# Kernel optimization log

Hardware: AMD Instinct MI355X
Metric: run time of the kernel (lower is better)

## Reference

```python
import jax, jax.numpy as jnp
import numpy as np

H, W, C, B = 96, 96, 21, 2
THETA_ALPHA, THETA_BETA, THETA_GAMMA = 160.0, 3.0, 3.0
N_ITERS = 5


def _coords():
    yy, xx = jnp.meshgrid(jnp.arange(H, dtype=jnp.float32),
                          jnp.arange(W, dtype=jnp.float32), indexing='ij')
    return jnp.stack([yy.ravel(), xx.ravel()], axis=-1)  # [N,2]


def _gauss_kernel(feat):
    # exact dense Gaussian kernel exp(-||fi-fj||^2/2); ground truth for the
    # permutohedral-lattice approximate high_dim_filter op.
    sq = jnp.sum(feat * feat, axis=-1)
    d2 = sq[:, None] + sq[None, :] - 2.0 * (feat @ feat.T)
    return jnp.exp(-0.5 * jnp.maximum(d2, 0.0))  # [N,N]


def setup_inputs():
    key = jax.random.key(0)
    k1, k2 = jax.random.split(key)
    unary = jax.random.normal(k1, (B, H, W, C), dtype=jnp.float32)
    rgb = jax.random.uniform(k2, (B, H, W, 3), dtype=jnp.float32) * 255.0
    return {
        'unary': unary,
        'rgb': rgb,
        'spatial_ker_weights': jnp.eye(C, dtype=jnp.float32),
        'bilateral_ker_weights': jnp.eye(C, dtype=jnp.float32),
        'compatibility_matrix': -jnp.eye(C, dtype=jnp.float32),
    }


def _crf_single(u_chw, rgb_chw, Ws, Wb, M):
    N = H * W
    pos = _coords()
    # filter op has no gradient w.r.t. guide features in the original custom op
    rgb_flat = jax.lax.stop_gradient(rgb_chw).reshape(3, N).T  # [N,3]
    Ks = _gauss_kernel(pos / THETA_GAMMA)                       # spatial kernel [N,N]
    Kb = _gauss_kernel(jnp.concatenate([pos / THETA_ALPHA,
                                        rgb_flat / THETA_BETA], axis=-1))  # bilateral [N,N]
    ones = jnp.ones((N,), dtype=jnp.float32)
    sn = Ks @ ones  # spatial norm vals (filter of all-ones)
    bn = Kb @ ones  # bilateral norm vals
    u = u_chw.reshape(C, N)
    q = u
    for _ in range(N_ITERS):
        sm = jax.nn.softmax(q, axis=0)   # softmax over classes, [C,N]
        sp = (sm @ Ks) / sn              # Ks symmetric -> filtering = sm @ Ks
        bl = (sm @ Kb) / bn
        msg = Ws @ sp + Wb @ bl          # learned message passing [C,N]
        q = u - M @ msg                  # compatibility transform + unary update
    return q  # [C,N]


def reference(unary, rgb, spatial_ker_weights, bilateral_ker_weights, compatibility_matrix):
    u = jnp.transpose(unary, (0, 3, 1, 2))  # [B,C,H,W]
    r = jnp.transpose(rgb, (0, 3, 1, 2))    # [B,3,H,W]
    q = jax.vmap(_crf_single, in_axes=(0, 0, None, None, None))(
        u, r, spatial_ker_weights, bilateral_ker_weights, compatibility_matrix)
    return jnp.transpose(q.reshape(B, C, H, W), (0, 2, 3, 1))  # [B,H,W,C]
```

## Files before the change

kernel.cpp:

```cpp
#include <hip/hip_runtime.h>

#define HH 96
#define WW 96
#define CC 21
#define BB 2
#define NN (HH*WW)
#define NT16 (NN/16)
#define NJB  (NN/32)
#define CHK 8
#define NCONV (BB*CC)
#define NBIL 648
#define PRUNE_T 24.0f
#define GST 104

#define KSA2 (0.84932184f / 160.0f)
#define KSB2 (0.84932184f / 3.0f)
#define GL2  (1.44269504f / 18.0f)

typedef __attribute__((ext_vector_type(4))) float f32x4;
typedef __attribute__((ext_vector_type(8))) short short8;
typedef __attribute__((ext_vector_type(4))) int int4v;

static __device__ inline unsigned pk_bf16(float a, float b) {
    unsigned ua = __builtin_bit_cast(unsigned, a);
    unsigned ub = __builtin_bit_cast(unsigned, b);
    ua += 0x7FFF + ((ua >> 16) & 1);
    ub += 0x7FFF + ((ub >> 16) & 1);
    return (ua >> 16) | (ub & 0xFFFF0000u);
}
static __device__ inline unsigned short bf16_1(float a) {
    unsigned ua = __builtin_bit_cast(unsigned, a);
    ua += 0x7FFF + ((ua >> 16) & 1);
    return (unsigned short)(ua >> 16);
}

__global__ __launch_bounds__(256) void histprep_kernel(
    const float* __restrict__ rgb, unsigned* __restrict__ gh,
    float* __restrict__ sxt, unsigned short* __restrict__ gbt,
    unsigned short* __restrict__ smht, unsigned* __restrict__ bnd)
{
    int tid = threadIdx.x;
    int gid = blockIdx.x * 256 + tid;
    if (gid < BB * NN) {
        int b = gid / NN;
        const float* rp = rgb + (size_t)gid * 3;
        int cr = min(15, (int)rp[0] >> 4);
        int cg = min(15, (int)rp[1] >> 4);
        int cb = min(15, (int)rp[2] >> 4);
        atomicAdd(&gh[b * 4096 + ((cr << 8) | (cg << 4) | cb)], 1u);
    }
    unsigned* smd = (unsigned*)smht;
    for (int o = gid; o < BB * 11 * (NN / 2); o += 104 * 256) {
        int b = o / (11 * (NN / 2));
        int rem = o - b * 11 * (NN / 2);
        int rr = rem / (NN / 2), col = rem - rr * (NN / 2);
        smd[(size_t)(b * 32 + 21 + rr) * (NN / 2) + col] = (rr == 0) ? 0x3F803F80u : 0u;
    }
    if (gid < BB * NT16 * 3) {
        int t2 = gid / 3, f = gid - t2 * 3;
        bnd[t2 * 6 + 2 * f + 1] = 0u;
    }
    if (blockIdx.x == 0) {
        __shared__ float gt[96];
        if (tid < 96) gt[tid] = __builtin_amdgcn_exp2f(-(float)(tid * tid) * GL2);
        __syncthreads();
        if (tid < 96) {
            float s = 0.f;
            for (int v = 0; v < 96; v++) s += gt[abs(tid - v)];
            sxt[tid] = s;
            for (int v = 0; v < 96; v++) gbt[tid * 96 + v] = bf16_1(gt[abs(tid - v)]);
        }
    }
}

__global__ __launch_bounds__(256) void scan_kernel(
    const unsigned* __restrict__ gh, int* __restrict__ goff,
    const unsigned* __restrict__ sent)
{
    __shared__ int ps[256];
    unsigned sv = sent[0];
    int t = threadIdx.x, b = blockIdx.x;
    int base = b * 4096 + t * 16;
    int loc[16], s = 0;
#pragma unroll
    for (int k = 0; k < 16; k++) { loc[k] = (int)(gh[base + k] - sv); s += loc[k]; }
    ps[t] = s;
    __syncthreads();
    for (int off = 1; off < 256; off <<= 1) {
        int add = (t >= off) ? ps[t - off] : 0;
        __syncthreads();
        ps[t] += add;
        __syncthreads();
    }
    int run = ps[t] - s;
#pragma unroll
    for (int k = 0; k < 16; k++) { goff[base + k] = run; run += loc[k]; }
}

__global__ __launch_bounds__(256) void scatter_kernel(
    const float* __restrict__ rgb, int* __restrict__ goff,
    int* __restrict__ spos, float* __restrict__ fjs, unsigned* __restrict__ bnd)
{
    int idx = blockIdx.x * 256 + threadIdx.x;
    if (idx >= BB * NN) return;
    int b = idx / NN, p = idx - b * NN;
    const float* rp = rgb + (size_t)idx * 3;
    float r = rp[0], g = rp[1], bl = rp[2];
    int cr = min(15, (int)r >> 4);
    int cg = min(15, (int)g >> 4);
    int cb = min(15, (int)bl >> 4);
    int pos = atomicAdd(&goff[b * 4096 + ((cr << 8) | (cg << 4) | cb)], 1);
    spos[idx] = pos;
    int y = p / WW, x = p - y * WW;
    float fr = r * KSB2, fg = g * KSB2, fb2 = bl * KSB2;
    float* fb = fjs + (size_t)b * 5 * NN;
    fb[0 * NN + pos] = fr;
    fb[1 * NN + pos] = fg;
    fb[2 * NN + pos] = fb2;
    fb[3 * NN + pos] = (float)y * KSA2;
    fb[4 * NN + pos] = (float)x * KSA2;
    unsigned* bq = bnd + (size_t)(b * NT16 + (pos >> 4)) * 6;
    atomicMin(&bq[0], __float_as_uint(fr));  atomicMax(&bq[1], __float_as_uint(fr));
    atomicMin(&bq[2], __float_as_uint(fg));  atomicMax(&bq[3], __float_as_uint(fg));
    atomicMin(&bq[4], __float_as_uint(fb2)); atomicMax(&bq[5], __float_as_uint(fb2));
}

__global__ __launch_bounds__(256) void masksoft_kernel(
    const float* __restrict__ bnd, unsigned short* __restrict__ jlist,
    int* __restrict__ cnt, int* __restrict__ wl, unsigned* __restrict__ wlc,
    const unsigned* __restrict__ sent,
    const float* __restrict__ q, const int* __restrict__ spos,
    unsigned short* __restrict__ smpb, unsigned short* __restrict__ smht,
    float* __restrict__ part)
{
    int tid = threadIdx.x;
    if (blockIdx.x < 288) {
        int lane = tid & 63;
        int bt = blockIdx.x * 4 + (tid >> 6);
        if (bt >= BB * NT16) return;
        int b = bt / NT16;
        const float* tb = bnd + (size_t)bt * 6;
        float tlo0 = tb[0], thi0 = tb[1], tlo1 = tb[2], thi1 = tb[3], tlo2 = tb[4], thi2 = tb[5];
        unsigned short* jl = jlist + (size_t)bt * NJB;
        const float* bb = bnd + (size_t)b * NT16 * 6;
        int n = 0;
#pragma unroll
        for (int r = 0; r < 5; r++) {
            int jb = r * 64 + lane;
            bool keep = false;
            if (jb < NJB) {
                const float* a0 = bb + (size_t)(2 * jb) * 6;
                float s = 0.f;
#pragma unroll
                for (int f = 0; f < 3; f++) {
                    float jlo = fminf(a0[2 * f], a0[6 + 2 * f]);
                    float jhi = fmaxf(a0[2 * f + 1], a0[6 + 2 * f + 1]);
                    float lo = (f == 0) ? tlo0 : (f == 1) ? tlo1 : tlo2;
                    float hi = (f == 0) ? thi0 : (f == 1) ? thi1 : thi2;
                    float gap = fmaxf(0.f, fmaxf(lo - jhi, jlo - hi));
                    s = fmaf(gap, gap, s);
                }
                keep = (s <= PRUNE_T);
            }
            unsigned long long m = __ballot(keep);
            if (keep) {
                int pre = __popcll(m & ((1ull << lane) - 1ull));
                jl[n + pre] = (unsigned short)jb;
            }
            n += __popcll(m);
        }
        if (lane == 0) {
            cnt[bt] = n;
            int nsl = (n + CHK - 1) / CHK;
            if (nsl > 0) {
                int base = (int)(atomicAdd(wlc, (unsigned)nsl) - sent[0]);
                for (int s2 = 0; s2 < nsl; s2++) wl[base + s2] = bt * 64 + s2;
            }
        }
        return;
    }
    int idx = (blockIdx.x - 288) * 256 + tid;
    if (idx >= BB * NN) return;
    int b = idx / NN, p = idx - b * NN;
    const float* qp = q + (size_t)idx * CC;
    float v[CC], m = -1e30f;
#pragma unroll
    for (int c = 0; c < CC; c++) { v[c] = qp[c]; m = fmaxf(m, v[c]); }
    float ssum = 0.f;
#pragma unroll
    for (int c = 0; c < CC; c++) { v[c] = __expf(v[c] - m); ssum += v[c]; }
    float inv = 1.0f / ssum;
    int s = spos[idx];
#pragma unroll
    for (int c = 0; c < CC; c++) {
        unsigned short h = bf16_1(v[c] * inv);
        smpb[(size_t)(b * CC + c) * NN + p] = h;
        smht[(size_t)(b * 32 + c) * NN + s] = h;
    }
    float* pp = part + (size_t)(b * NN + s) * 24;
#pragma unroll
    for (int k = 0; k < 24; k++) pp[k] = 0.f;
}

struct JSet { float vf[5][8]; short8 sb0, sb1; };

static __device__ __forceinline__ void load_jset(
    JSet& s, const float* __restrict__ fb, const unsigned short* __restrict__ smb,
    int jb, int quad, int l16)
{
    int coff = jb * 32 + quad * 8;
#pragma unroll
    for (int f = 0; f < 5; f++) {
        const float4* pf = (const float4*)(fb + (size_t)f * NN + coff);
        float4 lo = pf[0], hi = pf[1];
        s.vf[f][0] = lo.x; s.vf[f][1] = lo.y; s.vf[f][2] = lo.z; s.vf[f][3] = lo.w;
        s.vf[f][4] = hi.x; s.vf[f][5] = hi.y; s.vf[f][6] = hi.z; s.vf[f][7] = hi.w;
    }
    s.sb0 = *(const short8*)(smb + (size_t)l16 * NN + coff);
    s.sb1 = *(const short8*)(smb + (size_t)(16 + l16) * NN + coff);
}

static __device__ __forceinline__ void compute_jset(
    const JSet& s, float fi0, float fi1, float fi2, float fi3, float fi4,
    f32x4& acc0, f32x4& acc1)
{
    float kf[8];
#pragma unroll
    for (int e = 0; e < 8; e++) {
        float d0 = s.vf[0][e] - fi0;
        float d1 = s.vf[1][e] - fi1;
        float d2 = s.vf[2][e] - fi2;
        float d3 = s.vf[3][e] - fi3;
        float d4 = s.vf[4][e] - fi4;
        float sm = d0 * d0;
        sm = fmaf(d1, d1, sm);
        sm = fmaf(d2, d2, sm);
        sm = fmaf(d3, d3, sm);
        sm = fmaf(d4, d4, sm);
        kf[e] = __builtin_amdgcn_exp2f(-sm);
    }
    int4v ap = { (int)pk_bf16(kf[0], kf[1]), (int)pk_bf16(kf[2], kf[3]),
                 (int)pk_bf16(kf[4], kf[5]), (int)pk_bf16(kf[6], kf[7]) };
    short8 afrag = __builtin_bit_cast(short8, ap);
    acc0 = __builtin_amdgcn_mfma_f32_16x16x32_bf16(afrag, s.sb0, acc0, 0, 0, 0);
    acc1 = __builtin_amdgcn_mfma_f32_16x16x32_bf16(afrag, s.sb1, acc1, 0, 0, 0);
}

__global__ __launch_bounds__(256) void conv_bil_kernel(
    const unsigned short* __restrict__ smpb, const unsigned short* __restrict__ gbt,
    const float* __restrict__ sxt, float* __restrict__ spf,
    const unsigned short* __restrict__ smht_c, const float* __restrict__ fjs,
    const unsigned short* __restrict__ jlist, const int* __restrict__ cntv,
    const int* __restrict__ wl, const unsigned* __restrict__ wlc,
    const unsigned* __restrict__ sent, float* __restrict__ part)
{
    __shared__ unsigned short C1t[96 * GST];
    int tid = threadIdx.x;
    int lane = tid & 63, w = tid >> 6;
    int quad = lane >> 4, l16 = lane & 15;
    int bid = blockIdx.x;

    if (bid < NCONV) {
        const unsigned short* plane = smpb + (size_t)bid * NN;
        for (int mt = w; mt < 6; mt += 4) {
            int m0 = mt * 16;
            short8 a[3];
#pragma unroll
            for (int kk = 0; kk < 3; kk++)
                a[kk] = *(const short8*)(plane + (size_t)(m0 + l16) * 96 + kk * 32 + quad * 8);
            f32x4 acc[6];
#pragma unroll
            for (int nt = 0; nt < 6; nt++) acc[nt] = (f32x4){0.f, 0.f, 0.f, 0.f};
#pragma unroll
            for (int nt = 0; nt < 6; nt++) {
#pragma unroll
                for (int kk = 0; kk < 3; kk++) {
                    short8 bf = *(const short8*)(gbt + (nt * 16 + l16) * 96 + kk * 32 + quad * 8);
                    acc[nt] = __builtin_amdgcn_mfma_f32_16x16x32_bf16(a[kk], bf, acc[nt], 0, 0, 0);
                }
            }
#pragma unroll
            for (int nt = 0; nt < 6; nt++) {
                unsigned* dst = (unsigned*)&C1t[(nt * 16 + l16) * GST + m0 + quad * 4];
                dst[0] = pk_bf16(acc[nt][0], acc[nt][1]);
                dst[1] = pk_bf16(acc[nt][2], acc[nt][3]);
            }
        }
        __syncthreads();
        float* outp = spf + (size_t)bid * NN;
        for (int mt = w; mt < 6; mt += 4) {
            int m0 = mt * 16;
            short8 a[3];
#pragma unroll
            for (int kk = 0; kk < 3; kk++)
                a[kk] = *(const short8*)(gbt + (m0 + l16) * 96 + kk * 32 + quad * 8);
            f32x4 acc[6];
#pragma unroll
            for (int nt = 0; nt < 6; nt++) acc[nt] = (f32x4){0.f, 0.f, 0.f, 0.f};
#pragma unroll
            for (int nt = 0; nt < 6; nt++) {
#pragma unroll
                for (int kk = 0; kk < 3; kk++) {
                    short8 bf = *(const short8*)&C1t[(nt * 16 + l16) * GST + kk * 32 + quad * 8];
                    acc[nt] = __builtin_amdgcn_mfma_f32_16x16x32_bf16(a[kk], bf, acc[nt], 0, 0, 0);
                }
            }
#pragma unroll
            for (int nt = 0; nt < 6; nt++) {
                int x = nt * 16 + l16;
                float sx = sxt[x];
#pragma unroll
                for (int r = 0; r < 4; r++) {
                    int y = m0 + quad * 4 + r;
                    float invn = __builtin_amdgcn_rcpf(sxt[y] * sx);
                    outp[y * 96 + x] = acc[nt][r] * invn;
                }
            }
        }
        return;
    }

    int nwl = (int)(wlc[0] - sent[0]);
    for (int widx = (bid - NCONV) * 4 + w; widx < nwl; widx += NBIL * 4) {
        int e = wl[widx];
        int bt = e >> 6, ck = e & 63;
        int cnt = min(cntv[bt] - ck * CHK, CHK);
        int b = bt / NT16, tile16 = bt - b * NT16;
        int i = tile16 * 16 + l16;
        const float* fb = fjs + (size_t)b * 5 * NN;
        float fi0 = fb[0 * NN + i], fi1 = fb[1 * NN + i], fi2 = fb[2 * NN + i];
        float fi3 = fb[3 * NN + i], fi4 = fb[4 * NN + i];
        f32x4 acc0 = {0.f, 0.f, 0.f, 0.f};
        f32x4 acc1 = {0.f, 0.f, 0.f, 0.f};
        const unsigned short* smb = smht_c + (size_t)b * 32 * NN;
        const unsigned short* jl = jlist + (size_t)bt * NJB + ck * CHK;
        JSet A, B;
        load_jset(A, fb, smb, jl[0], quad, l16);
        int k = 0;
        while (true) {
            if (k + 1 < cnt) load_jset(B, fb, smb, jl[k + 1], quad, l16);
            compute_jset(A, fi0, fi1, fi2, fi3, fi4, acc0, acc1);
            if (++k >= cnt) break;
            if (k + 1 < cnt) load_jset(A, fb, smb, jl[k + 1], quad, l16);
            compute_jset(B, fi0, fi1, fi2, fi3, fi4, acc0, acc1);
            if (++k >= cnt) break;
        }
        int ibase = tile16 * 16 + quad * 4;
        float* pr = part + (size_t)b * NN * 24;
#pragma unroll
        for (int r = 0; r < 4; r++)
            atomicAdd(&pr[(size_t)(ibase + r) * 24 + l16], acc0[r]);
        if (l16 < 6) {
#pragma unroll
            for (int r = 0; r < 4; r++)
                atomicAdd(&pr[(size_t)(ibase + r) * 24 + 16 + l16], acc1[r]);
        }
    }
}

__global__ __launch_bounds__(128) void update_fused_kernel(
    const float* __restrict__ u, const float* __restrict__ spf,
    float* __restrict__ part, const int* __restrict__ spos,
    const float* __restrict__ Ws, const float* __restrict__ Wb,
    const float* __restrict__ M, float* __restrict__ qout,
    unsigned short* __restrict__ smpb, unsigned short* __restrict__ smht, int wr)
{
    __shared__ float sWs[441], sWb[441], sM[441];
    for (int t = threadIdx.x; t < 441; t += 128) {
        sWs[t] = Ws[t]; sWb[t] = Wb[t]; sM[t] = M[t];
    }
    __syncthreads();
    int idx = blockIdx.x * 128 + threadIdx.x;
    if (idx >= BB * NN) return;
    int b = idx / NN, p = idx - b * NN;
    int s = spos[idx];
    float* pp = part + (size_t)(b * NN + s) * 24;
    float blv[22];
#pragma unroll
    for (int c = 0; c < 22; c++) blv[c] = pp[c];
    float ninv = 1.0f / blv[21];
    float spv[CC], msg[CC];
#pragma unroll
    for (int c = 0; c < CC; c++) {
        blv[c] *= ninv;
        spv[c] = spf[(size_t)(b * CC + c) * NN + p];
    }
#pragma unroll
    for (int c = 0; c < CC; c++) {
        float a = 0.f;
        const float* wr2 = &sWs[c * CC];
        const float* br = &sWb[c * CC];
#pragma unroll
        for (int c2 = 0; c2 < CC; c2++) a = fmaf(wr2[c2], spv[c2], a);
#pragma unroll
        for (int c2 = 0; c2 < CC; c2++) a = fmaf(br[c2], blv[c2], a);
        msg[c] = a;
    }
    const float* up = u + (size_t)idx * CC;
    float qv[CC];
#pragma unroll
    for (int c = 0; c < CC; c++) {
        float a = up[c];
        const float* mr = &sM[c * CC];
#pragma unroll
        for (int c2 = 0; c2 < CC; c2++) a = fmaf(-mr[c2], msg[c2], a);
        qv[c] = a;
    }
    if (wr) {
        float m = -1e30f;
#pragma unroll
        for (int c = 0; c < CC; c++) m = fmaxf(m, qv[c]);
        float ssum = 0.f;
        float ev[CC];
#pragma unroll
        for (int c = 0; c < CC; c++) { ev[c] = __expf(qv[c] - m); ssum += ev[c]; }
        float inv = 1.0f / ssum;
#pragma unroll
        for (int c = 0; c < CC; c++) {
            unsigned short h = bf16_1(ev[c] * inv);
            smpb[(size_t)(b * CC + c) * NN + p] = h;
            smht[(size_t)(b * 32 + c) * NN + s] = h;
        }
#pragma unroll
        for (int k = 0; k < 24; k++) pp[k] = 0.f;
    } else {
        float* qp = qout + (size_t)idx * CC;
#pragma unroll
        for (int c = 0; c < CC; c++) qp[c] = qv[c];
    }
}

extern "C" void kernel_launch(void* const* d_in, const int* in_sizes, int n_in,
                              void* d_out, int out_size, void* d_ws, size_t ws_size,
                              hipStream_t stream)
{
    const float* unary = (const float*)d_in[0];
    const float* rgb   = (const float*)d_in[1];
    const float* Ws    = (const float*)d_in[2];
    const float* Wb    = (const float*)d_in[3];
    const float* M     = (const float*)d_in[4];
    float* out = (float*)d_out;

    float* SXT  = (float*)d_ws;
    float* FJS  = SXT + 96;
    float* SPF  = FJS + (size_t)BB * 5 * NN;
    float* PART = SPF + (size_t)BB * CC * NN;
    unsigned* BND = (unsigned*)(PART + (size_t)BB * NN * 24);
    int*   SPOS = (int*)(BND + (size_t)BB * NT16 * 6);
    unsigned* GH = (unsigned*)(SPOS + BB * NN);
    int*   GOFF = (int*)(GH + BB * 4096);
    int*   CNT  = GOFF + BB * 4096;
    unsigned* WLC = (unsigned*)(CNT + BB * NT16);
    unsigned* SENT = WLC + 1;
    int*   WL   = (int*)(SENT + 1);
    unsigned short* JL = (unsigned short*)(WL + BB * NT16 * 36);
    unsigned short* SMHT = JL + (size_t)BB * NT16 * NJB;
    unsigned short* SMPB = SMHT + (size_t)BB * 32 * NN;
    unsigned short* GBT  = SMPB + (size_t)BB * CC * NN;

    histprep_kernel<<<104, 256, 0, stream>>>(rgb, GH, SXT, GBT, SMHT, BND);
    scan_kernel<<<BB, 256, 0, stream>>>(GH, GOFF, SENT);
    scatter_kernel<<<(BB * NN + 255) / 256, 256, 0, stream>>>(rgb, GOFF, SPOS, FJS, BND);
    masksoft_kernel<<<360, 256, 0, stream>>>((const float*)BND, JL, CNT, WL, WLC, SENT,
                                             unary, SPOS, SMPB, SMHT, PART);
    for (int it = 0; it < 5; ++it) {
        conv_bil_kernel<<<NCONV + NBIL, 256, 0, stream>>>(
            SMPB, GBT, SXT, SPF, SMHT, FJS, JL, CNT, WL, WLC, SENT, PART);
        update_fused_kernel<<<(BB * NN + 127) / 128, 128, 0, stream>>>(
            unary, SPF, PART, SPOS, Ws, Wb, M, out, SMPB, SMHT, (it < 4) ? 1 : 0);
    }
}
```

Baseline: 309.4 us.

## Fuse histogram scan into scatter kernel and lower pruning threshold

Merges the scan and scatter kernels into one launch. Each scatter block redundantly scans its batch's 4096-bin histogram into shared memory. Slot assignment now comes from atomic decrements on a second histogram copy, so histprep builds two copies. Separately, the bilateral pruning threshold is lowered, which skips more tiles but loosens accuracy and risks tolerance failure.

```diff
diff --git a/kernel.cpp b/kernel.cpp
--- a/kernel.cpp
+++ b/kernel.cpp
@@ -10,7 +10,7 @@
 #define CHK 8
 #define NCONV (BB*CC)
 #define NBIL 648
-#define PRUNE_T 24.0f
+#define PRUNE_T 20.0f
 #define GST 104
 
 #define KSA2 (0.84932184f / 160.0f)
@@ -35,9 +35,10 @@
 }
 
 __global__ __launch_bounds__(256) void histprep_kernel(
-    const float* __restrict__ rgb, unsigned* __restrict__ gh,
-    float* __restrict__ sxt, unsigned short* __restrict__ gbt,
-    unsigned short* __restrict__ smht, unsigned* __restrict__ bnd)
+    const float* __restrict__ rgb, unsigned* __restrict__ gha,
+    unsigned* __restrict__ ghb, float* __restrict__ sxt,
+    unsigned short* __restrict__ gbt, unsigned short* __restrict__ smht,
+    unsigned* __restrict__ bnd)
 {
     int tid = threadIdx.x;
     int gid = blockIdx.x * 256 + tid;
@@ -47,7 +48,9 @@
         int cr = min(15, (int)rp[0] >> 4);
         int cg = min(15, (int)rp[1] >> 4);
         int cb = min(15, (int)rp[2] >> 4);
-        atomicAdd(&gh[b * 4096 + ((cr << 8) | (cg << 4) | cb)], 1u);
+        int cell = b * 4096 + ((cr << 8) | (cg << 4) | cb);
+        atomicAdd(&gha[cell], 1u);
+        atomicAdd(&ghb[cell], 1u);
     }
     unsigned* smd = (unsigned*)smht;
     for (int o = gid; o < BB * 11 * (NN / 2); o += 104 * 256) {
@@ -73,17 +76,21 @@
     }
 }
 
-__global__ __launch_bounds__(256) void scan_kernel(
-    const unsigned* __restrict__ gh, int* __restrict__ goff,
-    const unsigned* __restrict__ sent)
-{
+__global__ __launch_bounds__(256) void scanscatter_kernel(
+    const float* __restrict__ rgb, const unsigned* __restrict__ gha,
+    unsigned* __restrict__ ghb, const unsigned* __restrict__ sent,
+    int* __restrict__ spos, float* __restrict__ fjs, unsigned* __restrict__ bnd)
+{
+    __shared__ int sOff[4096];
     __shared__ int ps[256];
     unsigned sv = sent[0];
-    int t = threadIdx.x, b = blockIdx.x;
+    int t = threadIdx.x;
+    int blk = blockIdx.x;
+    int b = blk / (36);
     int base = b * 4096 + t * 16;
     int loc[16], s = 0;
 #pragma unroll
-    for (int k = 0; k < 16; k++) { loc[k] = (int)(gh[base + k] - sv); s += loc[k]; }
+    for (int k = 0; k < 16; k++) { loc[k] = (int)(gha[base + k] - sv); s += loc[k]; }
     ps[t] = s;
     __syncthreads();
     for (int off = 1; off < 256; off <<= 1) {
@@ -94,22 +101,18 @@
     }
     int run = ps[t] - s;
 #pragma unroll
-    for (int k = 0; k < 16; k++) { goff[base + k] = run; run += loc[k]; }
-}
-
-__global__ __launch_bounds__(256) void scatter_kernel(
-    const float* __restrict__ rgb, int* __restrict__ goff,
-    int* __restrict__ spos, float* __restrict__ fjs, unsigned* __restrict__ bnd)
-{
-    int idx = blockIdx.x * 256 + threadIdx.x;
-    if (idx >= BB * NN) return;
-    int b = idx / NN, p = idx - b * NN;
+    for (int k = 0; k < 16; k++) { sOff[t * 16 + k] = run; run += loc[k]; }
+    __syncthreads();
+    int idx = blk * 256 + t;
+    int p = idx - b * NN;
     const float* rp = rgb + (size_t)idx * 3;
     float r = rp[0], g = rp[1], bl = rp[2];
     int cr = min(15, (int)r >> 4);
     int cg = min(15, (int)g >> 4);
     int cb = min(15, (int)bl >> 4);
-    int pos = atomicAdd(&goff[b * 4096 + ((cr << 8) | (cg << 4) | cb)], 1);
+    int cell = (cr << 8) | (cg << 4) | cb;
+    unsigned old = atomicSub(&ghb[b * 4096 + cell], 1u);
+    int pos = sOff[cell] + (int)(old - sv) - 1;
     spos[idx] = pos;
     int y = p / WW, x = p - y * WW;
     float fr = r * KSB2, fg = g * KSB2, fb2 = bl * KSB2;
@@ -447,9 +450,9 @@
     float* PART = SPF + (size_t)BB * CC * NN;
     unsigned* BND = (unsigned*)(PART + (size_t)BB * NN * 24);
     int*   SPOS = (int*)(BND + (size_t)BB * NT16 * 6);
-    unsigned* GH = (unsigned*)(SPOS + BB * NN);
-    int*   GOFF = (int*)(GH + BB * 4096);
-    int*   CNT  = GOFF + BB * 4096;
+    unsigned* GHA = (unsigned*)(SPOS + BB * NN);
+    unsigned* GHB = GHA + BB * 4096;
+    int*   CNT  = (int*)(GHB + BB * 4096);
     unsigned* WLC = (unsigned*)(CNT + BB * NT16);
     unsigned* SENT = WLC + 1;
     int*   WL   = (int*)(SENT + 1);
@@ -458,9 +461,8 @@
     unsigned short* SMPB = SMHT + (size_t)BB * 32 * NN;
     unsigned short* GBT  = SMPB + (size_t)BB * CC * NN;
 
-    histprep_kernel<<<104, 256, 0, stream>>>(rgb, GH, SXT, GBT, SMHT, BND);
-    scan_kernel<<<BB, 256, 0, stream>>>(GH, GOFF, SENT);
-    scatter_kernel<<<(BB * NN + 255) / 256, 256, 0, stream>>>(rgb, GOFF, SPOS, FJS, BND);
+    histprep_kernel<<<104, 256, 0, stream>>>(rgb, GHA, GHB, SXT, GBT, SMHT, BND);
+    scanscatter_kernel<<<BB * 36, 256, 0, stream>>>(rgb, GHA, GHB, SENT, SPOS, FJS, BND);
     masksoft_kernel<<<360, 256, 0, stream>>>((const float*)BND, JL, CNT, WL, WLC, SENT,
                                              unary, SPOS, SMPB, SMHT, PART);
     for (int it = 0; it < 5; ++it) {
```

Measured after the change: 296.9 us. 1.04x faster.
